# Performance work log

Measured on AMD Instinct MI355X. Metric: run time of the kernel, lower is better.

The kernel has to match this reference:

```python
import jax, jax.numpy as jnp
import numpy as np

NUM_HEADS = 16
NUM_HIDDENS = 1024
D_K = NUM_HIDDENS // NUM_HEADS
NEG_INF = -1.0e9


def setup_inputs() -> dict:
    key = jax.random.key(0)
    kx, kq, kk, kv, ko, kl = jax.random.split(key, 6)
    B, S, D = 2, 2048, NUM_HIDDENS
    scale = 1.0 / np.sqrt(D)
    return {
        "X": jax.random.normal(kx, (B, S, D), dtype=jnp.float32),
        "valid_lens": jax.random.randint(kl, (B,), 0, S, dtype=jnp.int64),
        "W_q": jax.random.normal(kq, (D, D), dtype=jnp.float32) * scale,
        "W_k": jax.random.normal(kk, (D, D), dtype=jnp.float32) * scale,
        "W_v": jax.random.normal(kv, (D, D), dtype=jnp.float32) * scale,
        "W_o": jax.random.normal(ko, (D, D), dtype=jnp.float32) * scale,
    }


def _split_heads(x):
    # [B, S, D] -> [B, H, S, d_k]
    B, S, _ = x.shape
    return x.reshape(B, S, NUM_HEADS, D_K).transpose(0, 2, 1, 3)


def reference(X, valid_lens, W_q, W_k, W_v, W_o):
    B, S, D = X.shape
    # nn.Linear(bias=False): y = x @ W.T  (W is [out, in])
    Q = _split_heads(jnp.einsum("bsd,ed->bse", X, W_q))  # [B,H,S,dk]
    K = _split_heads(jnp.einsum("bsd,ed->bse", X, W_k))
    V = _split_heads(jnp.einsum("bsd,ed->bse", X, W_v))

    scores = jnp.einsum("bhqd,bhkd->bhqk", Q, K) / jnp.sqrt(
        jnp.asarray(D_K, dtype=X.dtype)
    )  # [B,H,S,S]

    # key-position mask per batch: positions >= valid_len get -1e9
    mask = jnp.arange(S)[None, :] >= valid_lens[:, None]  # [B,S]
    scores = jnp.where(mask[:, None, None, :], jnp.asarray(NEG_INF, X.dtype), scores)

    attn = jax.nn.softmax(scores, axis=-1)  # dropout p=0 -> identity
    out = jnp.einsum("bhqk,bhkd->bhqd", attn, V)  # [B,H,S,dk]
    out = out.transpose(0, 2, 1, 3).reshape(B, S, D)
    return jnp.einsum("bsd,ed->bse", out, W_o)
```

## Files before the change

### kernel.cpp

```cpp
#include <hip/hip_runtime.h>
#include <stdint.h>

#define S_LEN 2048
#define BATCH 2
#define DMODEL 1024
#define NHEAD 16
#define DK 64
#define MROWS (BATCH * S_LEN)

typedef __attribute__((ext_vector_type(8))) short bf16x8;
typedef __attribute__((ext_vector_type(4))) float f32x4;
typedef __attribute__((ext_vector_type(16))) float f32x16;
typedef __attribute__((ext_vector_type(4))) short short4v;

#define VMCNT(N) asm volatile("s_waitcnt vmcnt(" #N ")" ::: "memory")

__device__ __forceinline__ short f2b(float f) {
    union { float f; uint32_t u; } c; c.f = f;
    uint32_t u = c.u;
    return (short)((u + 0x7fffu + ((u >> 16) & 1u)) >> 16);
}

__device__ __forceinline__ void gload16(const void* g, void* l) {
    __builtin_amdgcn_global_load_lds(
        (const __attribute__((address_space(1))) void*)g,
        (__attribute__((address_space(3))) void*)l, 16, 0, 0);
}

__global__ void cvt_kernel(const float* __restrict__ X, const float* __restrict__ Wq,
                           const float* __restrict__ Wk, const float* __restrict__ Wv,
                           const float* __restrict__ Wo,
                           short* __restrict__ Xb, short* __restrict__ Wqb,
                           short* __restrict__ Wkb, short* __restrict__ Wvb,
                           short* __restrict__ Wob) {
    const float* src; short* dst; int n4;
    switch (blockIdx.y) {
        case 0:  src = X;  dst = Xb;  n4 = MROWS * DMODEL / 4;  break;
        case 1:  src = Wq; dst = Wqb; n4 = DMODEL * DMODEL / 4; break;
        case 2:  src = Wk; dst = Wkb; n4 = DMODEL * DMODEL / 4; break;
        case 3:  src = Wv; dst = Wvb; n4 = DMODEL * DMODEL / 4; break;
        default: src = Wo; dst = Wob; n4 = DMODEL * DMODEL / 4; break;
    }
    for (int i = blockIdx.x * blockDim.x + threadIdx.x; i < n4;
         i += gridDim.x * blockDim.x) {
        float4 v = ((const float4*)src)[i];
        short4v o;
        o[0] = f2b(v.x); o[1] = f2b(v.y); o[2] = f2b(v.z); o[3] = f2b(v.w);
        ((short4v*)dst)[i] = o;
    }
}

template <int OUT_F32>
__global__ __launch_bounds__(256) void gemm_bt(
    const short* __restrict__ A,
    const short* __restrict__ Bt0, const short* __restrict__ Bt1,
    const short* __restrict__ Bt2,
    short* __restrict__ Cb0, short* __restrict__ Cb1, short* __restrict__ Cb2,
    float* __restrict__ Cf, const int* __restrict__ vlens, int M, int N, int K) {
    __shared__ short sA[3][128 * 32];
    __shared__ short sB[3][128 * 32];

    const short* Bt = Bt0;
    short* Cb = Cb0;
    if (blockIdx.z == 1) { Bt = Bt1; Cb = Cb1; }
    else if (blockIdx.z == 2) { Bt = Bt2; Cb = Cb2; }

    const int brow = blockIdx.y * 128;
    if (!OUT_F32 && blockIdx.z >= 1 && vlens) {
        int vlb = vlens[brow >> 11];
        if (vlb <= 0 || vlb > S_LEN) vlb = S_LEN;
        else vlb = (vlb + 63) & ~63;
        if ((brow & (S_LEN - 1)) >= vlb) return;
    }

    const int tid = threadIdx.x;
    const int lane = tid & 63;
    const int wid = tid >> 6;
    const int wr = wid >> 1, wc = wid & 1;
    const int bcol = blockIdx.x * 128;
    const int lr = lane & 15;
    const int kh = (lane >> 4) << 3;
    const int swg = ((lr >> 1) & 3) << 3;
    const int khs = kh ^ swg;

    f32x4 acc[4][4] = {};

    const int idx0 = tid, idx1 = tid + 256;
    const int ar0 = idx0 >> 2, ak0 = ((idx0 & 3) << 3) ^ (((ar0 >> 1) & 3) << 3);
    const int ar1 = idx1 >> 2, ak1 = ((idx1 & 3) << 3) ^ (((ar1 >> 1) & 3) << 3);

    const short* gA0 = A + (size_t)(brow + ar0) * K + ak0;
    const short* gA1 = A + (size_t)(brow + ar1) * K + ak1;
    const short* gB0 = Bt + (size_t)(bcol + ar0) * K + ak0;
    const short* gB1 = Bt + (size_t)(bcol + ar1) * K + ak1;

#define G_STAGE(KT, PA, PB)                                   \
    do {                                                      \
        const int k0_ = (KT) << 5;                            \
        gload16(gA0 + k0_, (PA) + idx0 * 8);                  \
        gload16(gA1 + k0_, (PA) + idx1 * 8);                  \
        gload16(gB0 + k0_, (PB) + idx0 * 8);                  \
        gload16(gB1 + k0_, (PB) + idx1 * 8);                  \
    } while (0)

    const int nk = K >> 5;
    short* pA0 = &sA[0][0]; short* pA1 = &sA[1][0]; short* pA2 = &sA[2][0];
    short* pB0 = &sB[0][0]; short* pB1 = &sB[1][0]; short* pB2 = &sB[2][0];

    G_STAGE(0, pA0, pB0);
    G_STAGE(1, pA1, pB1);

    for (int kt = 0; kt < nk; ++kt) {
        if (kt == nk - 1) { VMCNT(0); } else { VMCNT(4); }
        __builtin_amdgcn_s_barrier();
        if (kt + 2 < nk) G_STAGE(kt + 2, pA2, pB2);

        bf16x8 a[4], b[4];
#pragma unroll
        for (int mt = 0; mt < 4; ++mt)
            a[mt] = *(const bf16x8*)&pA0[(wr * 64 + mt * 16 + lr) * 32 + khs];
#pragma unroll
        for (int nt = 0; nt < 4; ++nt)
            b[nt] = *(const bf16x8*)&pB0[(wc * 64 + nt * 16 + lr) * 32 + khs];
        __builtin_amdgcn_s_setprio(1);
#pragma unroll
        for (int mt = 0; mt < 4; ++mt)
#pragma unroll
            for (int nt = 0; nt < 4; ++nt)
                acc[mt][nt] = __builtin_amdgcn_mfma_f32_16x16x32_bf16(
                    a[mt], b[nt], acc[mt][nt], 0, 0, 0);
        __builtin_amdgcn_s_setprio(0);

        short* tA = pA0; pA0 = pA1; pA1 = pA2; pA2 = tA;
        short* tB = pB0; pB0 = pB1; pB1 = pB2; pB2 = tB;
    }
#undef G_STAGE

    const int rbase = (lane >> 4) << 2;
    const bool vtrans = (!OUT_F32) && (blockIdx.z == 2);
#pragma unroll
    for (int mt = 0; mt < 4; ++mt) {
#pragma unroll
        for (int nt = 0; nt < 4; ++nt) {
            if (vtrans) {
                int row0 = brow + wr * 64 + mt * 16 + rbase;
                int col = bcol + wc * 64 + nt * 16 + lr;
                int bb = row0 >> 11, key = row0 & 2047;
                int hh = col >> 6, d = col & 63;
                short4v pk;
#pragma unroll
                for (int j = 0; j < 4; ++j) pk[j] = f2b(acc[mt][nt][j]);
                *(short4v*)&Cb[((size_t)((bb * 16 + hh) * 64 + d)) * S_LEN + key] = pk;
            } else {
#pragma unroll
                for (int j = 0; j < 4; ++j) {
                    int row = brow + wr * 64 + mt * 16 + rbase + j;
                    int col = bcol + wc * 64 + nt * 16 + lr;
                    if (OUT_F32)
                        Cf[(size_t)row * N + col] = acc[mt][nt][j];
                    else
                        Cb[(size_t)row * N + col] = f2b(acc[mt][nt][j]);
                }
            }
        }
    }
}

__global__ __launch_bounds__(256, 2) void attn_kernel(
    const short* __restrict__ Q, const short* __restrict__ K,
    const short* __restrict__ Vt, short* __restrict__ O,
    const int* __restrict__ vlens) {
    __shared__ short sK[4][64 * 64];
    __shared__ short sV[4][64 * 64];

    const int tid = threadIdx.x;
    const int lane = tid & 63;
    const int w = tid >> 6;
    const int id = blockIdx.x;
    const int xcd = id & 7;
    const int r = id >> 3;
    const int b = (r >> 5) & 1;
    const int h = (xcd << 1) | (r & 1);
    const int qb = (r >> 1) & 15;
    const int rl_ = lane & 31;
    const int g = lane >> 5;

    int vl = vlens[b];
    if (vl < 0) vl = 0;
    if (vl > S_LEN) vl = S_LEN;
    const bool allm = (vl == 0);
    if (allm) vl = S_LEN;
    const int nT = (vl + 63) >> 6;
    const int nFull = ((vl & 63) == 0) ? nT : nT - 1;

    const size_t rowbase = (size_t)(b * S_LEN) * DMODEL + h * DK;
    const short* vt = Vt + ((size_t)((b * 16 + h) * 64)) * S_LEN;

    const int q = qb * 128 + w * 32 + rl_;
    const short* qA = Q + rowbase + (size_t)q * DMODEL;
    bf16x8 qf[4];
#pragma unroll
    for (int f = 0; f < 4; ++f)
        qf[f] = *(const bf16x8*)(qA + f * 16 + g * 8);
    if (allm) {
#pragma unroll
        for (int f = 0; f < 4; ++f)
#pragma unroll
            for (int i = 0; i < 8; ++i) qf[f][i] = 0;
    }

    f32x16 oac0 = {}, oac1 = {};
    float m_run = -1e30f, mc = -1e30f, l_run = 0.f;
    const float CEXP = 0.18033688011112042f;
    const float THRADD = 44.361419556f;

    const int rsw = (((rl_ & 7) ^ ((rl_ >> 3) & 3)) << 3);
    int lofs[4];
#pragma unroll
    for (int f = 0; f < 4; ++f)
        lofs[f] = rl_ * 64 + ((f * 16 + g * 8) ^ rsw);

    const int kr = tid >> 3;
    const int kc = (((tid & 7) ^ (kr & 7) ^ ((kr >> 3) & 3)) << 3);
    const short* kBase = K + rowbase + (size_t)kr * DMODEL + kc;
    const short* vBase = vt + (size_t)kr * S_LEN + kc;

    short* const sK0 = &sK[0][0];
    short* const sV0 = &sV[0][0];
#define KBUF(i) (sK0 + (i) * 4096)
#define VBUF(i) (sV0 + (i) * 4096)

#define A_STAGE(T, PK, PV)                                                      \
    do {                                                                        \
        const short* kg_ = kBase + (size_t)((T) * 64) * DMODEL;                 \
        gload16(kg_, (PK) + tid * 8);                                           \
        gload16(kg_ + (size_t)32 * DMODEL, (PK) + (tid + 256) * 8);             \
        const short* vg_ = vBase + (T) * 64;                                    \
        gload16(vg_, (PV) + tid * 8);                                           \
        gload16(vg_ + (size_t)32 * S_LEN, (PV) + (tid + 256) * 8);              \
    } while (0)

#define MK_FRAG(A0, A1, A2, A3)                                                 \
    ({ union { uint32_t u[4]; bf16x8 v; } _f;                                   \
       _f.u[0] = (A0); _f.u[1] = (A1); _f.u[2] = (A2); _f.u[3] = (A3); _f.v; })

#define TILE_BODY(MASKED_C, PK, PV)                                             \
    do {                                                                        \
        constexpr bool MASKED = MASKED_C;                                       \
        f32x16 s0 = {}, s1 = {};                                                \
        __builtin_amdgcn_s_setprio(1);                                          \
        _Pragma("unroll")                                                       \
        for (int f = 0; f < 4; ++f) {                                           \
            bf16x8 ka = *(const bf16x8*)&(PK)[lofs[f]];                         \
            bf16x8 kb2 = *(const bf16x8*)&(PK)[lofs[f] + 2048];                 \
            s0 = __builtin_amdgcn_mfma_f32_32x32x16_bf16(ka, qf[f], s0, 0, 0, 0); \
            s1 = __builtin_amdgcn_mfma_f32_32x32x16_bf16(kb2, qf[f], s1, 0, 0, 0); \
        }                                                                       \
        __builtin_amdgcn_s_setprio(0);                                          \
        if (MASKED) {                                                           \
            _Pragma("unroll")                                                   \
            for (int rg = 0; rg < 16; ++rg) {                                   \
                int key0 = t * 64 + (rg & 3) + 8 * (rg >> 2) + 4 * g;           \
                if (key0 >= vl) s0[rg] = -3.0e38f;                              \
                if (key0 + 32 >= vl) s1[rg] = -3.0e38f;                         \
            }                                                                   \
        }                                                                       \
        float x0 = fmaxf(fmaxf(s0[0], s0[1]), fmaxf(s0[2], s0[3]));             \
        float x1 = fmaxf(fmaxf(s0[4], s0[5]), fmaxf(s0[6], s0[7]));             \
        float x2 = fmaxf(fmaxf(s0[8], s0[9]), fmaxf(s0[10], s0[11]));           \
        float x3 = fmaxf(fmaxf(s0[12], s0[13]), fmaxf(s0[14], s0[15]));         \
        float x4 = fmaxf(fmaxf(s1[0], s1[1]), fmaxf(s1[2], s1[3]));             \
        float x5 = fmaxf(fmaxf(s1[4], s1[5]), fmaxf(s1[6], s1[7]));             \
        float x6 = fmaxf(fmaxf(s1[8], s1[9]), fmaxf(s1[10], s1[11]));           \
        float x7 = fmaxf(fmaxf(s1[12], s1[13]), fmaxf(s1[14], s1[15]));         \
        float px = fmaxf(fmaxf(fmaxf(x0, x1), fmaxf(x2, x3)),                   \
                         fmaxf(fmaxf(x4, x5), fmaxf(x6, x7)));                  \
        if (__any(px > m_run + THRADD)) {                                       \
            float mx = fmaxf(px, __shfl_xor(px, 32));                           \
            mx = fmaxf(mx, m_run);                                              \
            float scl = __builtin_exp2f((m_run - mx) * CEXP);                   \
            m_run = mx; mc = mx * CEXP;                                         \
            l_run *= scl;                                                       \
            _Pragma("unroll")                                                   \
            for (int i = 0; i < 16; ++i) { oac0[i] *= scl; oac1[i] *= scl; }    \
        }                                                                       \
        uint32_t P0[8], P1[8];                                                  \
        float ls = 0.f;                                                         \
        _Pragma("unroll")                                                       \
        for (int i = 0; i < 8; ++i) {                                           \
            float a0 = __builtin_exp2f(__builtin_fmaf(s0[2 * i], CEXP, -mc));   \
            float a1 = __builtin_exp2f(__builtin_fmaf(s0[2 * i + 1], CEXP, -mc)); \
            float b0 = __builtin_exp2f(__builtin_fmaf(s1[2 * i], CEXP, -mc));   \
            float b1 = __builtin_exp2f(__builtin_fmaf(s1[2 * i + 1], CEXP, -mc)); \
            ls += (a0 + a1) + (b0 + b1);                                        \
            asm("v_cvt_pk_bf16_f32 %0, %1, %2" : "=v"(P0[i]) : "v"(a0), "v"(a1)); \
            asm("v_cvt_pk_bf16_f32 %0, %1, %2" : "=v"(P1[i]) : "v"(b0), "v"(b1)); \
        }                                                                       \
        l_run += ls;                                                            \
        asm volatile("v_permlane32_swap_b32 %0, %1" : "+v"(P0[0]), "+v"(P0[2])); \
        asm volatile("v_permlane32_swap_b32 %0, %1" : "+v"(P0[1]), "+v"(P0[3])); \
        asm volatile("v_permlane32_swap_b32 %0, %1" : "+v"(P0[4]), "+v"(P0[6])); \
        asm volatile("v_permlane32_swap_b32 %0, %1" : "+v"(P0[5]), "+v"(P0[7])); \
        asm volatile("v_permlane32_swap_b32 %0, %1" : "+v"(P1[0]), "+v"(P1[2])); \
        asm volatile("v_permlane32_swap_b32 %0, %1" : "+v"(P1[1]), "+v"(P1[3])); \
        asm volatile("v_permlane32_swap_b32 %0, %1" : "+v"(P1[4]), "+v"(P1[6])); \
        asm volatile("v_permlane32_swap_b32 %0, %1" : "+v"(P1[5]), "+v"(P1[7])); \
        bf16x8 F0 = MK_FRAG(P0[0], P0[1], P0[2], P0[3]);                        \
        bf16x8 F1 = MK_FRAG(P0[4], P0[5], P0[6], P0[7]);                        \
        bf16x8 F2 = MK_FRAG(P1[0], P1[1], P1[2], P1[3]);                        \
        bf16x8 F3 = MK_FRAG(P1[4], P1[5], P1[6], P1[7]);                        \
        __builtin_amdgcn_s_setprio(1);                                          \
        {                                                                       \
            bf16x8 v0 = *(const bf16x8*)&(PV)[lofs[0]];                         \
            bf16x8 v1 = *(const bf16x8*)&(PV)[lofs[0] + 2048];                  \
            oac0 = __builtin_amdgcn_mfma_f32_32x32x16_bf16(v0, F0, oac0, 0, 0, 0); \
            oac1 = __builtin_amdgcn_mfma_f32_32x32x16_bf16(v1, F0, oac1, 0, 0, 0); \
            v0 = *(const bf16x8*)&(PV)[lofs[1]];                                \
            v1 = *(const bf16x8*)&(PV)[lofs[1] + 2048];                         \
            oac0 = __builtin_amdgcn_mfma_f32_32x32x16_bf16(v0, F1, oac0, 0, 0, 0); \
            oac1 = __builtin_amdgcn_mfma_f32_32x32x16_bf16(v1, F1, oac1, 0, 0, 0); \
            v0 = *(const bf16x8*)&(PV)[lofs[2]];                                \
            v1 = *(const bf16x8*)&(PV)[lofs[2] + 2048];                         \
            oac0 = __builtin_amdgcn_mfma_f32_32x32x16_bf16(v0, F2, oac0, 0, 0, 0); \
            oac1 = __builtin_amdgcn_mfma_f32_32x32x16_bf16(v1, F2, oac1, 0, 0, 0); \
            v0 = *(const bf16x8*)&(PV)[lofs[3]];                                \
            v1 = *(const bf16x8*)&(PV)[lofs[3] + 2048];                         \
            oac0 = __builtin_amdgcn_mfma_f32_32x32x16_bf16(v0, F3, oac0, 0, 0, 0); \
            oac1 = __builtin_amdgcn_mfma_f32_32x32x16_bf16(v1, F3, oac1, 0, 0, 0); \
        }                                                                       \
        __builtin_amdgcn_s_setprio(0);                                          \
    } while (0)

    A_STAGE(0, KBUF(0), VBUF(0));
    if (nT > 1) A_STAGE(1, KBUF(1), VBUF(1));
    if (nT > 2) A_STAGE(2, KBUF(2), VBUF(2));

    for (int t = 0; t < nT; ++t) {
        const int rem = nT - 1 - t;
        if (rem >= 2) { VMCNT(8); }
        else if (rem == 1) { VMCNT(4); }
        else { VMCNT(0); }
        __builtin_amdgcn_s_barrier();
        if (t + 3 < nT) A_STAGE(t + 3, KBUF((t + 3) & 3), VBUF((t + 3) & 3));

        short* curK = KBUF(t & 3);
        short* curV = VBUF(t & 3);
        if (t < nFull) TILE_BODY(false, curK, curV);
        else TILE_BODY(true, curK, curV);
    }
#undef TILE_BODY
#undef A_STAGE
#undef MK_FRAG
#undef KBUF
#undef VBUF

    float lt = l_run + __shfl_xor(l_run, 32);
    float rl2 = 1.f / lt;

    short* orow = O + rowbase + (size_t)q * DMODEL;
#pragma unroll
    for (int r2 = 0; r2 < 4; ++r2) {
        short4v pk0, pk1;
#pragma unroll
        for (int j = 0; j < 4; ++j) {
            pk0[j] = f2b(oac0[r2 * 4 + j] * rl2);
            pk1[j] = f2b(oac1[r2 * 4 + j] * rl2);
        }
        int d0 = r2 * 8 + 4 * g;
        *(short4v*)&orow[d0] = pk0;
        *(short4v*)&orow[32 + d0] = pk1;
    }
}

extern "C" void kernel_launch(void* const* d_in, const int* in_sizes, int n_in,
                              void* d_out, int out_size, void* d_ws, size_t ws_size,
                              hipStream_t stream) {
    const float* X = (const float*)d_in[0];
    const int* vlens = (const int*)d_in[1];
    const float* Wq = (const float*)d_in[2];
    const float* Wk = (const float*)d_in[3];
    const float* Wv = (const float*)d_in[4];
    const float* Wo = (const float*)d_in[5];
    float* out = (float*)d_out;

    short* Xb = (short*)d_ws;
    short* Wqb = Xb + (size_t)MROWS * DMODEL;
    short* Wkb = Wqb + (size_t)DMODEL * DMODEL;
    short* Wvb = Wkb + (size_t)DMODEL * DMODEL;
    short* Wob = Wvb + (size_t)DMODEL * DMODEL;
    short* Qb = Wob + (size_t)DMODEL * DMODEL;
    short* Kb = Qb + (size_t)MROWS * DMODEL;
    short* Vtb = Kb + (size_t)MROWS * DMODEL;
    short* Ob = Vtb + (size_t)MROWS * DMODEL;

    cvt_kernel<<<dim3(512, 5), 256, 0, stream>>>(X, Wq, Wk, Wv, Wo, Xb, Wqb, Wkb,
                                                 Wvb, Wob);
    gemm_bt<0><<<dim3(8, 32, 3), 256, 0, stream>>>(Xb, Wqb, Wkb, Wvb, Qb, Kb, Vtb,
                                                   nullptr, vlens, MROWS, DMODEL,
                                                   DMODEL);
    attn_kernel<<<dim3(512), 256, 0, stream>>>(Qb, Kb, Vtb, Ob, vlens);
    gemm_bt<1><<<dim3(8, 32, 1), 256, 0, stream>>>(Ob, Wob, Wob, Wob, nullptr,
                                                   nullptr, nullptr, out, nullptr,
                                                   MROWS, DMODEL, DMODEL);
}
```

Measured before the change: 102.2 us.

## Software-pipeline attention so QK of tile t overlaps PV of tile t-1

Splits the per-tile body into a QK MFMA phase, a softmax phase and a PV MFMA phase. Each iteration now issues QK for the current tile together with PV for the previous tile, carrying the bf16 P fragments across iterations, with a final PV after the loop. The goal is to let matrix-core work overlap the softmax VALU/transcendental work and shorten serial dependency chains. The K/V LDS ring grows from 4 to 5 stages so the previous V tile stays resident, which raises LDS use to 80KB per block and may limit occupancy.

After: 101.9 us, median of 3. About the same (-0.3%).

```diff
diff --git a/kernel.cpp b/kernel.cpp
--- a/kernel.cpp
+++ b/kernel.cpp
@@ -170,8 +170,8 @@
     const short* __restrict__ Q, const short* __restrict__ K,
     const short* __restrict__ Vt, short* __restrict__ O,
     const int* __restrict__ vlens) {
-    __shared__ short sK[4][64 * 64];
-    __shared__ short sV[4][64 * 64];
+    __shared__ short sK[5][64 * 64];
+    __shared__ short sV[5][64 * 64];
 
     const int tid = threadIdx.x;
     const int lane = tid & 63;
@@ -244,19 +244,31 @@
     ({ union { uint32_t u[4]; bf16x8 v; } _f;                                   \
        _f.u[0] = (A0); _f.u[1] = (A1); _f.u[2] = (A2); _f.u[3] = (A3); _f.v; })
 
-#define TILE_BODY(MASKED_C, PK, PV)                                             \
+    bf16x8 pF0 = {}, pF1 = {}, pF2 = {}, pF3 = {};
+
+#define PV_BODY(PV)                                                             \
+    do {                                                                        \
+        bf16x8 v0 = *(const bf16x8*)&(PV)[lofs[0]];                             \
+        bf16x8 v1 = *(const bf16x8*)&(PV)[lofs[0] + 2048];                      \
+        oac0 = __builtin_amdgcn_mfma_f32_32x32x16_bf16(v0, pF0, oac0, 0, 0, 0); \
+        oac1 = __builtin_amdgcn_mfma_f32_32x32x16_bf16(v1, pF0, oac1, 0, 0, 0); \
+        v0 = *(const bf16x8*)&(PV)[lofs[1]];                                    \
+        v1 = *(const bf16x8*)&(PV)[lofs[1] + 2048];                             \
+        oac0 = __builtin_amdgcn_mfma_f32_32x32x16_bf16(v0, pF1, oac0, 0, 0, 0); \
+        oac1 = __builtin_amdgcn_mfma_f32_32x32x16_bf16(v1, pF1, oac1, 0, 0, 0); \
+        v0 = *(const bf16x8*)&(PV)[lofs[2]];                                    \
+        v1 = *(const bf16x8*)&(PV)[lofs[2] + 2048];                             \
+        oac0 = __builtin_amdgcn_mfma_f32_32x32x16_bf16(v0, pF2, oac0, 0, 0, 0); \
+        oac1 = __builtin_amdgcn_mfma_f32_32x32x16_bf16(v1, pF2, oac1, 0, 0, 0); \
+        v0 = *(const bf16x8*)&(PV)[lofs[3]];                                    \
+        v1 = *(const bf16x8*)&(PV)[lofs[3] + 2048];                             \
+        oac0 = __builtin_amdgcn_mfma_f32_32x32x16_bf16(v0, pF3, oac0, 0, 0, 0); \
+        oac1 = __builtin_amdgcn_mfma_f32_32x32x16_bf16(v1, pF3, oac1, 0, 0, 0); \
+    } while (0)
+
+#define SM_BODY(MASKED_C)                                                       \
     do {                                                                        \
         constexpr bool MASKED = MASKED_C;                                       \
-        f32x16 s0 = {}, s1 = {};                                                \
-        __builtin_amdgcn_s_setprio(1);                                          \
-        _Pragma("unroll")                                                       \
-        for (int f = 0; f < 4; ++f) {                                           \
-            bf16x8 ka = *(const bf16x8*)&(PK)[lofs[f]];                         \
-            bf16x8 kb2 = *(const bf16x8*)&(PK)[lofs[f] + 2048];                 \
-            s0 = __builtin_amdgcn_mfma_f32_32x32x16_bf16(ka, qf[f], s0, 0, 0, 0); \
-            s1 = __builtin_amdgcn_mfma_f32_32x32x16_bf16(kb2, qf[f], s1, 0, 0, 0); \
-        }                                                                       \
-        __builtin_amdgcn_s_setprio(0);                                          \
         if (MASKED) {                                                           \
             _Pragma("unroll")                                                   \
             for (int rg = 0; rg < 16; ++rg) {                                   \
@@ -305,50 +317,51 @@
         asm volatile("v_permlane32_swap_b32 %0, %1" : "+v"(P1[1]), "+v"(P1[3])); \
         asm volatile("v_permlane32_swap_b32 %0, %1" : "+v"(P1[4]), "+v"(P1[6])); \
         asm volatile("v_permlane32_swap_b32 %0, %1" : "+v"(P1[5]), "+v"(P1[7])); \
-        bf16x8 F0 = MK_FRAG(P0[0], P0[1], P0[2], P0[3]);                        \
-        bf16x8 F1 = MK_FRAG(P0[4], P0[5], P0[6], P0[7]);                        \
-        bf16x8 F2 = MK_FRAG(P1[0], P1[1], P1[2], P1[3]);                        \
-        bf16x8 F3 = MK_FRAG(P1[4], P1[5], P1[6], P1[7]);                        \
-        __builtin_amdgcn_s_setprio(1);                                          \
-        {                                                                       \
-            bf16x8 v0 = *(const bf16x8*)&(PV)[lofs[0]];                         \
-            bf16x8 v1 = *(const bf16x8*)&(PV)[lofs[0] + 2048];                  \
-            oac0 = __builtin_amdgcn_mfma_f32_32x32x16_bf16(v0, F0, oac0, 0, 0, 0); \
-            oac1 = __builtin_amdgcn_mfma_f32_32x32x16_bf16(v1, F0, oac1, 0, 0, 0); \
-            v0 = *(const bf16x8*)&(PV)[lofs[1]];                                \
-            v1 = *(const bf16x8*)&(PV)[lofs[1] + 2048];                         \
-            oac0 = __builtin_amdgcn_mfma_f32_32x32x16_bf16(v0, F1, oac0, 0, 0, 0); \
-            oac1 = __builtin_amdgcn_mfma_f32_32x32x16_bf16(v1, F1, oac1, 0, 0, 0); \
-            v0 = *(const bf16x8*)&(PV)[lofs[2]];                                \
-            v1 = *(const bf16x8*)&(PV)[lofs[2] + 2048];                         \
-            oac0 = __builtin_amdgcn_mfma_f32_32x32x16_bf16(v0, F2, oac0, 0, 0, 0); \
-            oac1 = __builtin_amdgcn_mfma_f32_32x32x16_bf16(v1, F2, oac1, 0, 0, 0); \
-            v0 = *(const bf16x8*)&(PV)[lofs[3]];                                \
-            v1 = *(const bf16x8*)&(PV)[lofs[3] + 2048];                         \
-            oac0 = __builtin_amdgcn_mfma_f32_32x32x16_bf16(v0, F3, oac0, 0, 0, 0); \
-            oac1 = __builtin_amdgcn_mfma_f32_32x32x16_bf16(v1, F3, oac1, 0, 0, 0); \
-        }                                                                       \
-        __builtin_amdgcn_s_setprio(0);                                          \
+        pF0 = MK_FRAG(P0[0], P0[1], P0[2], P0[3]);                              \
+        pF1 = MK_FRAG(P0[4], P0[5], P0[6], P0[7]);                              \
+        pF2 = MK_FRAG(P1[0], P1[1], P1[2], P1[3]);                              \
+        pF3 = MK_FRAG(P1[4], P1[5], P1[6], P1[7]);                              \
     } while (0)
 
     A_STAGE(0, KBUF(0), VBUF(0));
     if (nT > 1) A_STAGE(1, KBUF(1), VBUF(1));
     if (nT > 2) A_STAGE(2, KBUF(2), VBUF(2));
 
+    int cur = 0, stg = 3, prv = 4;
     for (int t = 0; t < nT; ++t) {
         const int rem = nT - 1 - t;
         if (rem >= 2) { VMCNT(8); }
         else if (rem == 1) { VMCNT(4); }
         else { VMCNT(0); }
         __builtin_amdgcn_s_barrier();
-        if (t + 3 < nT) A_STAGE(t + 3, KBUF((t + 3) & 3), VBUF((t + 3) & 3));
-
-        short* curK = KBUF(t & 3);
-        short* curV = VBUF(t & 3);
-        if (t < nFull) TILE_BODY(false, curK, curV);
-        else TILE_BODY(true, curK, curV);
-    }
-#undef TILE_BODY
+        if (t + 3 < nT) A_STAGE(t + 3, KBUF(stg), VBUF(stg));
+
+        const short* PK = KBUF(cur);
+        f32x16 s0 = {}, s1 = {};
+        __builtin_amdgcn_s_setprio(1);
+#pragma unroll
+        for (int f = 0; f < 4; ++f) {
+            bf16x8 ka = *(const bf16x8*)&PK[lofs[f]];
+            bf16x8 kb2 = *(const bf16x8*)&PK[lofs[f] + 2048];
+            s0 = __builtin_amdgcn_mfma_f32_32x32x16_bf16(ka, qf[f], s0, 0, 0, 0);
+            s1 = __builtin_amdgcn_mfma_f32_32x32x16_bf16(kb2, qf[f], s1, 0, 0, 0);
+        }
+        if (t > 0) PV_BODY(VBUF(prv));
+        __builtin_amdgcn_s_setprio(0);
+
+        if (t < nFull) SM_BODY(false);
+        else SM_BODY(true);
+
+        prv = cur;
+        cur = (cur == 4) ? 0 : cur + 1;
+        stg = (stg == 4) ? 0 : stg + 1;
+    }
+    __builtin_amdgcn_s_setprio(1);
+    PV_BODY(VBUF(prv));
+    __builtin_amdgcn_s_setprio(0);
+
+#undef SM_BODY
+#undef PV_BODY
 #undef A_STAGE
 #undef MK_FRAG
 #undef KBUF
```

## Split attention into 64-query blocks of two waves with triple-buffered K/V

Applied to the files above, without the earlier changes.

The attention kernel now runs 1024 workgroups of 128 threads, each handling 64 queries instead of 128, and the block-index decode is remapped to match. The K/V prefetch ring drops from four stages to three, prefetching two tiles ahead, and each thread issues four 16-byte loads per matrix per tile. The aim is better load balance across CUs when valid lengths are short, and lower LDS use per block so more blocks fit. In exchange, each K/V tile is fetched by twice as many workgroups, which adds memory traffic, and the shallower prefetch may expose more load latency.

After: 123.6 us. 1.21x slower.

```diff
diff --git a/kernel.cpp b/kernel.cpp
--- a/kernel.cpp
+++ b/kernel.cpp
@@ -166,22 +166,22 @@
     }
 }
 
-__global__ __launch_bounds__(256, 2) void attn_kernel(
+__global__ __launch_bounds__(128, 3) void attn_kernel(
     const short* __restrict__ Q, const short* __restrict__ K,
     const short* __restrict__ Vt, short* __restrict__ O,
     const int* __restrict__ vlens) {
-    __shared__ short sK[4][64 * 64];
-    __shared__ short sV[4][64 * 64];
+    __shared__ short sK[3][64 * 64];
+    __shared__ short sV[3][64 * 64];
 
     const int tid = threadIdx.x;
     const int lane = tid & 63;
     const int w = tid >> 6;
     const int id = blockIdx.x;
     const int xcd = id & 7;
-    const int r = id >> 3;
-    const int b = (r >> 5) & 1;
-    const int h = (xcd << 1) | (r & 1);
-    const int qb = (r >> 1) & 15;
+    const int rr = id >> 3;
+    const int b = rr & 1;
+    const int h = (xcd << 1) | ((rr >> 1) & 1);
+    const int qb = rr >> 2;
     const int rl_ = lane & 31;
     const int g = lane >> 5;
 
@@ -196,7 +196,7 @@
     const size_t rowbase = (size_t)(b * S_LEN) * DMODEL + h * DK;
     const short* vt = Vt + ((size_t)((b * 16 + h) * 64)) * S_LEN;
 
-    const int q = qb * 128 + w * 32 + rl_;
+    const int q = qb * 64 + w * 32 + rl_;
     const short* qA = Q + rowbase + (size_t)q * DMODEL;
     bf16x8 qf[4];
 #pragma unroll
@@ -220,10 +220,13 @@
     for (int f = 0; f < 4; ++f)
         lofs[f] = rl_ * 64 + ((f * 16 + g * 8) ^ rsw);
 
-    const int kr = tid >> 3;
-    const int kc = (((tid & 7) ^ (kr & 7) ^ ((kr >> 3) & 3)) << 3);
-    const short* kBase = K + rowbase + (size_t)kr * DMODEL + kc;
-    const short* vBase = vt + (size_t)kr * S_LEN + kc;
+    const int kr0 = tid >> 3;
+    int kcs[4];
+#pragma unroll
+    for (int i = 0; i < 4; ++i) {
+        int rw = kr0 + 16 * i;
+        kcs[i] = (((tid & 7) ^ (rw & 7) ^ ((rw >> 3) & 3)) << 3);
+    }
 
     short* const sK0 = &sK[0][0];
     short* const sV0 = &sV[0][0];
@@ -232,12 +235,16 @@
 
 #define A_STAGE(T, PK, PV)                                                      \
     do {                                                                        \
-        const short* kg_ = kBase + (size_t)((T) * 64) * DMODEL;                 \
-        gload16(kg_, (PK) + tid * 8);                                           \
-        gload16(kg_ + (size_t)32 * DMODEL, (PK) + (tid + 256) * 8);             \
-        const short* vg_ = vBase + (T) * 64;                                    \
-        gload16(vg_, (PV) + tid * 8);                                           \
-        gload16(vg_ + (size_t)32 * S_LEN, (PV) + (tid + 256) * 8);              \
+        const short* kg_ = K + rowbase + (size_t)((T) * 64) * DMODEL;           \
+        const short* vg_ = vt + (T) * 64;                                       \
+        _Pragma("unroll")                                                       \
+        for (int i_ = 0; i_ < 4; ++i_) {                                        \
+            int rw_ = kr0 + 16 * i_;                                            \
+            gload16(kg_ + (size_t)rw_ * DMODEL + kcs[i_],                       \
+                    (PK) + (tid + 128 * i_) * 8);                               \
+            gload16(vg_ + (size_t)rw_ * S_LEN + kcs[i_],                        \
+                    (PV) + (tid + 128 * i_) * 8);                               \
+        }                                                                       \
     } while (0)
 
 #define MK_FRAG(A0, A1, A2, A3)                                                 \
@@ -333,20 +340,19 @@
 
     A_STAGE(0, KBUF(0), VBUF(0));
     if (nT > 1) A_STAGE(1, KBUF(1), VBUF(1));
-    if (nT > 2) A_STAGE(2, KBUF(2), VBUF(2));
-
+
+    int cur = 0, stg = 2;
     for (int t = 0; t < nT; ++t) {
         const int rem = nT - 1 - t;
-        if (rem >= 2) { VMCNT(8); }
-        else if (rem == 1) { VMCNT(4); }
-        else { VMCNT(0); }
+        if (rem >= 1) { VMCNT(8); } else { VMCNT(0); }
         __builtin_amdgcn_s_barrier();
-        if (t + 3 < nT) A_STAGE(t + 3, KBUF((t + 3) & 3), VBUF((t + 3) & 3));
-
-        short* curK = KBUF(t & 3);
-        short* curV = VBUF(t & 3);
-        if (t < nFull) TILE_BODY(false, curK, curV);
-        else TILE_BODY(true, curK, curV);
+        if (t + 2 < nT) A_STAGE(t + 2, KBUF(stg), VBUF(stg));
+
+        if (t < nFull) TILE_BODY(false, KBUF(cur), VBUF(cur));
+        else TILE_BODY(true, KBUF(cur), VBUF(cur));
+
+        cur = (cur == 2) ? 0 : cur + 1;
+        stg = (stg == 2) ? 0 : stg + 1;
     }
 #undef TILE_BODY
 #undef A_STAGE
@@ -398,7 +404,7 @@
     gemm_bt<0><<<dim3(8, 32, 3), 256, 0, stream>>>(Xb, Wqb, Wkb, Wvb, Qb, Kb, Vtb,
                                                    nullptr, vlens, MROWS, DMODEL,
                                                    DMODEL);
-    attn_kernel<<<dim3(512), 256, 0, stream>>>(Qb, Kb, Vtb, Ob, vlens);
+    attn_kernel<<<dim3(1024), 128, 0, stream>>>(Qb, Kb, Vtb, Ob, vlens);
     gemm_bt<1><<<dim3(8, 32, 1), 256, 0, stream>>>(Ob, Wob, Wob, Wob, nullptr,
                                                    nullptr, nullptr, out, nullptr,
                                                    MROWS, DMODEL, DMODEL);
```
